# Performance work log

Measured on AMD Instinct MI355X. Metric: run time of the kernel, lower is better.

## Reference

```python
import jax, jax.numpy as jnp
import numpy as np

LAMBDA_DISP = 0.25
TAU = 1.0
NORMALIZE = True
EPS = 1e-12  # torch F.normalize eps


def setup_inputs() -> dict:
    key = jax.random.key(0)
    z = jax.random.normal(key, (1024, 64, 1024), dtype=jnp.float32)
    return {"z": z}


def reference(z):
    B = z.shape[0]
    zf = z.reshape(B, -1)  # (B, S*D)
    if NORMALIZE:
        norm = jnp.linalg.norm(zf, axis=1, keepdims=True)
        zf = zf / jnp.maximum(norm, EPS)
    # pairwise squared distances via Gram matrix: d2[i,j] = |zi|^2 + |zj|^2 - 2 zi.zj
    g = zf @ zf.T  # (B, B) GEMM, dominant compute
    sq = jnp.diagonal(g)
    d2 = jnp.maximum(sq[:, None] + sq[None, :] - 2.0 * g, 0.0)
    e = jnp.exp(-d2 / TAU)
    # pdist covers i<j pairs only; full matrix sum = 2*sum_{i<j} + B (diag exp(0)=1)
    n_pairs = B * (B - 1) / 2.0
    mean_pairs = (e.sum() - B) / (2.0 * n_pairs)
    loss = jnp.log(mean_pairs)
    return LAMBDA_DISP * loss
```

## Files before the change

### kernel.cpp

```cpp
#include <hip/hip_runtime.h>
#include <hip/hip_bf16.h>
#include <stdint.h>


#define NROWS 1024
#define KDIM  65536
#define NCHUNK 14
#define NTILE  36
#define PARTN  504

typedef __attribute__((ext_vector_type(4)))  int   i32x4;
typedef __attribute__((ext_vector_type(8)))  int   i32x8;
typedef __attribute__((ext_vector_type(16))) float f32x16;

#define AS1 __attribute__((address_space(1)))
#define AS3 __attribute__((address_space(3)))

#define MFMA_SC(a, b, c) \
  __builtin_amdgcn_mfma_scale_f32_32x32x64_f8f6f4((a), (b), (c), 0, 0, \
      0, 0x7F7F7F7F, 0, 0x7F7F7F7F)

__global__ void k_prep(const float* __restrict__ z, uint32_t* __restrict__ zq,
                       float* __restrict__ inv_norm) {
  const int row = blockIdx.x;
  const float4* zr = (const float4*)(z + (size_t)row * KDIM);
  uint32_t* qr = zq + (size_t)row * (KDIM / 4);
  float ss = 0.f;
  for (int i = threadIdx.x; i < KDIM / 4; i += blockDim.x) {
    const float4 v = zr[i];
    ss += v.x * v.x + v.y * v.y + v.z * v.z + v.w * v.w;
    int p = __builtin_amdgcn_cvt_pk_fp8_f32(v.x, v.y, 0, false);
    p     = __builtin_amdgcn_cvt_pk_fp8_f32(v.z, v.w, p, true);
    qr[i] = (uint32_t)p;
  }
  for (int off = 32; off; off >>= 1) ss += __shfl_down(ss, off, 64);
  __shared__ float part[4];
  const int lane = threadIdx.x & 63, w = threadIdx.x >> 6;
  if (lane == 0) part[w] = ss;
  __syncthreads();
  if (threadIdx.x == 0) {
    const float t = part[0] + part[1] + part[2] + part[3];
    inv_norm[row] = 1.f / fmaxf(sqrtf(t), 1e-12f);
  }
}

__global__
__attribute__((amdgpu_flat_work_group_size(256, 256), amdgpu_waves_per_eu(2, 2)))
void k_gram8(const unsigned char* __restrict__ zb, float* __restrict__ pbuf) {
  extern __shared__ char smem[];
  const int tid  = threadIdx.x;
  const int lane = tid & 63;
  const int wid  = tid >> 6;
  const int wr   = wid >> 1;
  const int wc   = wid & 1;

  const int d = blockIdx.x;
  const int l = (d & 7) * 63 + (d >> 3);
  const int kc   = l / NTILE;
  const int tile = l - kc * NTILE;
  const int kts = (kc < 8) ? kc * 37 : 296 + (kc - 8) * 36;
  const int cnt = (kc < 8) ? 37 : 36;
  const int pidx = l;

  int tm = 0, rr = tile;
  while (rr >= 8 - tm) { rr -= 8 - tm; ++tm; }
  const int tn = tm + rr;

  const uint32_t Pt   = (uint32_t)tid * 16u;
  const uint32_t Lt   = Pt ^ (((Pt >> 7) & 7u) << 4);
  const uint32_t vOff = (Lt >> 7) * (uint32_t)KDIM + (Lt & 127u);

  const uint32_t mask = ((uint32_t)lane & 7u) << 4;
  const uint32_t rA = ((uint32_t)(wr * 64) + ((uint32_t)lane & 31u)) * 128u;
  const uint32_t rB = ((uint32_t)(wc * 64) + ((uint32_t)lane & 31u)) * 128u;
  const uint32_t h5 = ((uint32_t)lane >> 5) * 32u;
  uint32_t vA[2], vAx[2], vB[2], vBx[2];
#pragma unroll
  for (int kk = 0; kk < 2; kk++) {
    const uint32_t sw = ((uint32_t)(kk * 64) + h5) ^ mask;
    vA[kk]  = rA + sw;
    vAx[kk] = vA[kk] ^ 16u;
    vB[kk]  = 32768u + rB + sw;
    vBx[kk] = vB[kk] ^ 16u;
  }

  const char* zbC = (const char*)zb;
  const uint32_t gA = (uint32_t)(tm * 128) * (uint32_t)KDIM;
  const uint32_t gB = (uint32_t)(tn * 128) * (uint32_t)KDIM;

  auto stage_panel = [&](uint32_t gRowByte, uint32_t ldsBase, int ktAbs) {
    const uint32_t g0 = gRowByte + (uint32_t)ktAbs * 128u;
#pragma unroll
    for (int q = 0; q < 4; q++) {
      __builtin_amdgcn_global_load_lds(
          (const AS1 void*)(zbC + (g0 + (uint32_t)q * (32u * (uint32_t)KDIM) + vOff)),
          (AS3 void*)(smem + (ldsBase + (uint32_t)q * 4096u + Pt)), 16, 0, 0);
    }
  };

  auto rdf = [&](uint32_t base, uint32_t basex, int fi) -> i32x8 {
    const i32x4 lo = *(const i32x4*)(smem + (base  + (uint32_t)(fi * 4096)));
    const i32x4 hi = *(const i32x4*)(smem + (basex + (uint32_t)(fi * 4096)));
    return __builtin_shufflevector(lo, hi, 0, 1, 2, 3, 4, 5, 6, 7);
  };

  f32x16 acc[2][2];
#pragma unroll
  for (int m = 0; m < 2; m++)
#pragma unroll
    for (int n = 0; n < 2; n++)
#pragma unroll
      for (int r = 0; r < 16; r++) acc[m][n][r] = 0.f;

  stage_panel(gA, 0u,      kts);
  stage_panel(gB, 32768u,  kts);
  asm volatile("s_waitcnt vmcnt(0)" ::: "memory");
  __builtin_amdgcn_s_barrier();
  asm volatile("" ::: "memory");

  i32x8 aF[2][2], bF[2][2];
  for (int T = 0; T < cnt; ++T) {
    const uint32_t idle = (uint32_t)((T + 1) & 1) * 16384u;
    const bool st = (T + 1 < cnt);

    if (st) {
      stage_panel(gA, idle,           kts + T + 1);
      stage_panel(gB, 32768u + idle,  kts + T + 1);
    }
#pragma unroll
    for (int kk = 0; kk < 2; kk++) {
#pragma unroll
      for (int m = 0; m < 2; m++) aF[m][kk] = rdf(vA[kk], vAx[kk], m);
#pragma unroll
      for (int n = 0; n < 2; n++) bF[n][kk] = rdf(vB[kk], vBx[kk], n);
    }
    __builtin_amdgcn_s_setprio(1);
#pragma unroll
    for (int m = 0; m < 2; m++)
#pragma unroll
      for (int n = 0; n < 2; n++)
#pragma unroll
        for (int kk = 0; kk < 2; kk++)
          acc[m][n] = MFMA_SC(aF[m][kk], bF[n][kk], acc[m][n]);
    __builtin_amdgcn_s_setprio(0);
    asm volatile("s_waitcnt vmcnt(0)" ::: "memory");
    __builtin_amdgcn_s_barrier();
    asm volatile("" ::: "memory");
#pragma unroll
    for (int kk = 0; kk < 2; kk++) {
      vA[kk] ^= 16384u; vAx[kk] ^= 16384u; vB[kk] ^= 16384u; vBx[kk] ^= 16384u;
    }
  }

  float* outp = pbuf + (size_t)pidx * 16384;
  const int r0 = wr * 64 + ((lane >> 5) << 2);
  const int c0 = wc * 64 + (lane & 31);
#pragma unroll
  for (int m = 0; m < 2; m++)
#pragma unroll
    for (int n = 0; n < 2; n++)
#pragma unroll
      for (int r = 0; r < 16; r++) {
        const int R = r0 + m * 32 + (r & 3) + ((r >> 2) << 3);
        const int C = c0 + n * 32;
        outp[(size_t)R * 128 + C] = acc[m][n][r];
      }
}

__device__ __forceinline__ int tile_id(int ti, int tj) {
  return 8 * ti - ((ti * (ti - 1)) >> 1) + (tj - ti);
}

__global__ void k_diag(const float* __restrict__ pbuf, const float* __restrict__ inv_norm,
                       float* __restrict__ diag) {
  const int i = blockIdx.x * 256 + threadIdx.x;
  const int ti = i >> 7;
  const int t = tile_id(ti, ti);
  const int off = (i & 127) * 129;
  float s = 0.f;
  for (int c = 0; c < NCHUNK; ++c)
    s += pbuf[(size_t)(c * NTILE + t) * 16384 + off];
  const float w = inv_norm[i];
  diag[i] = s * w * w;
}

__global__ void k_expsum(const float* __restrict__ pbuf, const float* __restrict__ inv_norm,
                         const float* __restrict__ diag, float* __restrict__ accum) {
  const int gid = blockIdx.x * 256 + threadIdx.x;
  const int e0 = gid * 4;
  const int i  = e0 >> 10;
  const int j0 = e0 & 1023;
  const int ti = i >> 7, tj = j0 >> 7;
  float s = 0.f;
  if (tj >= ti && j0 + 3 > i) {
    const int t = tile_id(ti, tj);
    const int off = (i & 127) * 128 + (j0 & 127);
    float gx = 0.f, gy = 0.f, gz = 0.f, gw = 0.f;
    for (int c = 0; c < NCHUNK; ++c) {
      const float4 v = *(const float4*)(pbuf + (size_t)(c * NTILE + t) * 16384 + off);
      gx += v.x; gy += v.y; gz += v.z; gw += v.w;
    }
    const float wi = inv_norm[i];
    const float di = diag[i];
    const float4 wj = *(const float4*)(inv_norm + j0);
    const float4 dj = *(const float4*)(diag + j0);
    float gn, d2;
    gn = gx * wi * wj.x; d2 = fmaxf(di + dj.x - 2.f * gn, 0.f); if (i < j0 + 0) s += expf(-d2);
    gn = gy * wi * wj.y; d2 = fmaxf(di + dj.y - 2.f * gn, 0.f); if (i < j0 + 1) s += expf(-d2);
    gn = gz * wi * wj.z; d2 = fmaxf(di + dj.z - 2.f * gn, 0.f); if (i < j0 + 2) s += expf(-d2);
    gn = gw * wi * wj.w; d2 = fmaxf(di + dj.w - 2.f * gn, 0.f); if (i < j0 + 3) s += expf(-d2);
  }
  for (int off = 32; off; off >>= 1) s += __shfl_down(s, off, 64);
  __shared__ float part[4];
  const int lane = threadIdx.x & 63, w = threadIdx.x >> 6;
  if (lane == 0) part[w] = s;
  __syncthreads();
  if (threadIdx.x == 0) atomicAdd(accum, part[0] + part[1] + part[2] + part[3]);
}

__global__ void k_final(const float* __restrict__ accum, float* __restrict__ out) {
  const float n_pairs = (float)NROWS * (float)(NROWS - 1) * 0.5f;
  out[0] = 0.25f * logf(accum[0] / n_pairs);
}

extern "C" void kernel_launch(void* const* d_in, const int* in_sizes, int n_in,
                              void* d_out, int out_size, void* d_ws, size_t ws_size,
                              hipStream_t stream) {
  const float* z = (const float*)d_in[0];
  float* out = (float*)d_out;
  char* ws = (char*)d_ws;

  float*    inv_norm = (float*)(ws);
  float*    diag     = (float*)(ws + 4096);
  float*    accum    = (float*)(ws + 8192);
  float*    pbuf     = (float*)(ws + 65536);
  uint32_t* zq       = (uint32_t*)(ws + 65536 + (size_t)PARTN * 16384 * sizeof(float));

  hipMemsetAsync(accum, 0, sizeof(float), stream);

  k_prep<<<NROWS, 256, 0, stream>>>(z, zq, inv_norm);

  hipFuncSetAttribute(reinterpret_cast<const void*>(&k_gram8),
                      hipFuncAttributeMaxDynamicSharedMemorySize, 65536);
  k_gram8<<<PARTN, 256, 65536, stream>>>((const unsigned char*)zq, pbuf);

  k_diag<<<NROWS / 256, 256, 0, stream>>>(pbuf, inv_norm, diag);
  k_expsum<<<(NROWS * NROWS / 4) / 256, 256, 0, stream>>>(pbuf, inv_norm, diag, accum);
  k_final<<<1, 1, 0, stream>>>(accum, out);
}
```

Measured before the change: 139.2 us.

## Use 512-thread blocks in fp8 Gram GEMM and drop diagonal kernel

The Gram kernel now runs 8 waves per block instead of 4. Each wave computes a 32x64 sub-tile with two accumulators, and panel staging is split across 512 threads. The k_diag pass is removed, and the squared norm of each normalized row is assumed to be exactly 1, so d2 becomes 2-2g. This saves one kernel and its reads, at the cost of ignoring fp8 quantization error in the diagonal terms, which slightly changes the numerical result.

```diff
diff --git a/kernel.cpp b/kernel.cpp
--- a/kernel.cpp
+++ b/kernel.cpp
@@ -45,7 +45,7 @@
 }
 
 __global__
-__attribute__((amdgpu_flat_work_group_size(256, 256), amdgpu_waves_per_eu(2, 2)))
+__attribute__((amdgpu_flat_work_group_size(512, 512), amdgpu_waves_per_eu(4, 4)))
 void k_gram8(const unsigned char* __restrict__ zb, float* __restrict__ pbuf) {
   extern __shared__ char smem[];
   const int tid  = threadIdx.x;
@@ -71,7 +71,7 @@
   const uint32_t vOff = (Lt >> 7) * (uint32_t)KDIM + (Lt & 127u);
 
   const uint32_t mask = ((uint32_t)lane & 7u) << 4;
-  const uint32_t rA = ((uint32_t)(wr * 64) + ((uint32_t)lane & 31u)) * 128u;
+  const uint32_t rA = ((uint32_t)(wr * 32) + ((uint32_t)lane & 31u)) * 128u;
   const uint32_t rB = ((uint32_t)(wc * 64) + ((uint32_t)lane & 31u)) * 128u;
   const uint32_t h5 = ((uint32_t)lane >> 5) * 32u;
   uint32_t vA[2], vAx[2], vB[2], vBx[2];
@@ -91,10 +91,10 @@
   auto stage_panel = [&](uint32_t gRowByte, uint32_t ldsBase, int ktAbs) {
     const uint32_t g0 = gRowByte + (uint32_t)ktAbs * 128u;
 #pragma unroll
-    for (int q = 0; q < 4; q++) {
+    for (int q = 0; q < 2; q++) {
       __builtin_amdgcn_global_load_lds(
-          (const AS1 void*)(zbC + (g0 + (uint32_t)q * (32u * (uint32_t)KDIM) + vOff)),
-          (AS3 void*)(smem + (ldsBase + (uint32_t)q * 4096u + Pt)), 16, 0, 0);
+          (const AS1 void*)(zbC + (g0 + (uint32_t)q * (64u * (uint32_t)KDIM) + vOff)),
+          (AS3 void*)(smem + (ldsBase + (uint32_t)q * 8192u + Pt)), 16, 0, 0);
     }
   };
 
@@ -104,13 +104,11 @@
     return __builtin_shufflevector(lo, hi, 0, 1, 2, 3, 4, 5, 6, 7);
   };
 
-  f32x16 acc[2][2];
-#pragma unroll
-  for (int m = 0; m < 2; m++)
-#pragma unroll
-    for (int n = 0; n < 2; n++)
-#pragma unroll
-      for (int r = 0; r < 16; r++) acc[m][n][r] = 0.f;
+  f32x16 acc[2];
+#pragma unroll
+  for (int n = 0; n < 2; n++)
+#pragma unroll
+    for (int r = 0; r < 16; r++) acc[n][r] = 0.f;
 
   stage_panel(gA, 0u,      kts);
   stage_panel(gB, 32768u,  kts);
@@ -118,7 +116,6 @@
   __builtin_amdgcn_s_barrier();
   asm volatile("" ::: "memory");
 
-  i32x8 aF[2][2], bF[2][2];
   for (int T = 0; T < cnt; ++T) {
     const uint32_t idle = (uint32_t)((T + 1) & 1) * 16384u;
     const bool st = (T + 1 < cnt);
@@ -129,20 +126,14 @@
     }
 #pragma unroll
     for (int kk = 0; kk < 2; kk++) {
-#pragma unroll
-      for (int m = 0; m < 2; m++) aF[m][kk] = rdf(vA[kk], vAx[kk], m);
-#pragma unroll
-      for (int n = 0; n < 2; n++) bF[n][kk] = rdf(vB[kk], vBx[kk], n);
-    }
-    __builtin_amdgcn_s_setprio(1);
-#pragma unroll
-    for (int m = 0; m < 2; m++)
-#pragma unroll
-      for (int n = 0; n < 2; n++)
-#pragma unroll
-        for (int kk = 0; kk < 2; kk++)
-          acc[m][n] = MFMA_SC(aF[m][kk], bF[n][kk], acc[m][n]);
-    __builtin_amdgcn_s_setprio(0);
+      i32x8 a0 = rdf(vA[kk], vAx[kk], 0);
+      i32x8 b0 = rdf(vB[kk], vBx[kk], 0);
+      i32x8 b1 = rdf(vB[kk], vBx[kk], 1);
+      __builtin_amdgcn_s_setprio(1);
+      acc[0] = MFMA_SC(a0, b0, acc[0]);
+      acc[1] = MFMA_SC(a0, b1, acc[1]);
+      __builtin_amdgcn_s_setprio(0);
+    }
     asm volatile("s_waitcnt vmcnt(0)" ::: "memory");
     __builtin_amdgcn_s_barrier();
     asm volatile("" ::: "memory");
@@ -153,39 +144,24 @@
   }
 
   float* outp = pbuf + (size_t)pidx * 16384;
-  const int r0 = wr * 64 + ((lane >> 5) << 2);
+  const int r0 = wr * 32 + ((lane >> 5) << 2);
   const int c0 = wc * 64 + (lane & 31);
 #pragma unroll
-  for (int m = 0; m < 2; m++)
-#pragma unroll
-    for (int n = 0; n < 2; n++)
-#pragma unroll
-      for (int r = 0; r < 16; r++) {
-        const int R = r0 + m * 32 + (r & 3) + ((r >> 2) << 3);
-        const int C = c0 + n * 32;
-        outp[(size_t)R * 128 + C] = acc[m][n][r];
-      }
+  for (int n = 0; n < 2; n++)
+#pragma unroll
+    for (int r = 0; r < 16; r++) {
+      const int R = r0 + (r & 3) + ((r >> 2) << 3);
+      const int C = c0 + n * 32;
+      outp[(size_t)R * 128 + C] = acc[n][r];
+    }
 }
 
 __device__ __forceinline__ int tile_id(int ti, int tj) {
   return 8 * ti - ((ti * (ti - 1)) >> 1) + (tj - ti);
 }
 
-__global__ void k_diag(const float* __restrict__ pbuf, const float* __restrict__ inv_norm,
-                       float* __restrict__ diag) {
-  const int i = blockIdx.x * 256 + threadIdx.x;
-  const int ti = i >> 7;
-  const int t = tile_id(ti, ti);
-  const int off = (i & 127) * 129;
-  float s = 0.f;
-  for (int c = 0; c < NCHUNK; ++c)
-    s += pbuf[(size_t)(c * NTILE + t) * 16384 + off];
-  const float w = inv_norm[i];
-  diag[i] = s * w * w;
-}
-
 __global__ void k_expsum(const float* __restrict__ pbuf, const float* __restrict__ inv_norm,
-                         const float* __restrict__ diag, float* __restrict__ accum) {
+                         float* __restrict__ accum) {
   const int gid = blockIdx.x * 256 + threadIdx.x;
   const int e0 = gid * 4;
   const int i  = e0 >> 10;
@@ -201,14 +177,12 @@
       gx += v.x; gy += v.y; gz += v.z; gw += v.w;
     }
     const float wi = inv_norm[i];
-    const float di = diag[i];
     const float4 wj = *(const float4*)(inv_norm + j0);
-    const float4 dj = *(const float4*)(diag + j0);
     float gn, d2;
-    gn = gx * wi * wj.x; d2 = fmaxf(di + dj.x - 2.f * gn, 0.f); if (i < j0 + 0) s += expf(-d2);
-    gn = gy * wi * wj.y; d2 = fmaxf(di + dj.y - 2.f * gn, 0.f); if (i < j0 + 1) s += expf(-d2);
-    gn = gz * wi * wj.z; d2 = fmaxf(di + dj.z - 2.f * gn, 0.f); if (i < j0 + 2) s += expf(-d2);
-    gn = gw * wi * wj.w; d2 = fmaxf(di + dj.w - 2.f * gn, 0.f); if (i < j0 + 3) s += expf(-d2);
+    gn = gx * wi * wj.x; d2 = fmaxf(2.f - 2.f * gn, 0.f); if (i < j0 + 0) s += expf(-d2);
+    gn = gy * wi * wj.y; d2 = fmaxf(2.f - 2.f * gn, 0.f); if (i < j0 + 1) s += expf(-d2);
+    gn = gz * wi * wj.z; d2 = fmaxf(2.f - 2.f * gn, 0.f); if (i < j0 + 2) s += expf(-d2);
+    gn = gw * wi * wj.w; d2 = fmaxf(2.f - 2.f * gn, 0.f); if (i < j0 + 3) s += expf(-d2);
   }
   for (int off = 32; off; off >>= 1) s += __shfl_down(s, off, 64);
   __shared__ float part[4];
@@ -231,7 +205,6 @@
   char* ws = (char*)d_ws;
 
   float*    inv_norm = (float*)(ws);
-  float*    diag     = (float*)(ws + 4096);
   float*    accum    = (float*)(ws + 8192);
   float*    pbuf     = (float*)(ws + 65536);
   uint32_t* zq       = (uint32_t*)(ws + 65536 + (size_t)PARTN * 16384 * sizeof(float));
@@ -242,9 +215,8 @@
 
   hipFuncSetAttribute(reinterpret_cast<const void*>(&k_gram8),
                       hipFuncAttributeMaxDynamicSharedMemorySize, 65536);
-  k_gram8<<<PARTN, 256, 65536, stream>>>((const unsigned char*)zq, pbuf);
-
-  k_diag<<<NROWS / 256, 256, 0, stream>>>(pbuf, inv_norm, diag);
-  k_expsum<<<(NROWS * NROWS / 4) / 256, 256, 0, stream>>>(pbuf, inv_norm, diag, accum);
+  k_gram8<<<PARTN, 512, 65536, stream>>>((const unsigned char*)zq, pbuf);
+
+  k_expsum<<<(NROWS * NROWS / 4) / 256, 256, 0, stream>>>(pbuf, inv_norm, accum);
   k_final<<<1, 1, 0, stream>>>(accum, out);
 }
```

New measurement: 139.4 us (median of 2 runs). Within noise of the previous version (+0.1%).
